# Optimization experiments

Hardware: AMD Instinct MI355X
Metric: run time of the kernel (lower is better)

## Reference

```python
import jax, jax.numpy as jnp
import numpy as np

N = 10000        # nodes
E = 160000       # edges
C = 128          # channel multiplicity (128x0e input)
RBF = 20         # edge_attr_dim
HID = 32         # edge MLP hidden
WN = 3 * C       # tp.weight_numel: 3 uvu paths (0e x Y_l -> l), 128 weights each


def setup_inputs() -> dict:
    key = jax.random.key(0)
    ks = jax.random.split(key, 12)
    f = lambda k, s, sc=1.0: jax.random.normal(k, s, jnp.float32) * sc
    return {
        "node_feat": f(ks[0], (N, C)),
        "edge_attr": f(ks[1], (E, RBF)),
        "edge_rsh": f(ks[2], (E, 9)),
        "edge_index": jax.random.randint(ks[3], (2, E), 0, N),
        # mlp_edge_scalar: Linear(2C->32), Linear(32->WN)
        "Ws1": f(ks[4], (2 * C, HID), 1.0 / np.sqrt(2 * C)), "bs1": jnp.zeros((HID,), jnp.float32),
        "Ws2": f(ks[5], (HID, WN), 1.0 / np.sqrt(HID)), "bs2": jnp.zeros((WN,), jnp.float32),
        # mlp_edge_rbf: Linear(20->32), Linear(32->WN)
        "Wr1": f(ks[6], (RBF, HID), 1.0 / np.sqrt(RBF)), "br1": jnp.zeros((HID,), jnp.float32),
        "Wr2": f(ks[7], (HID, WN), 1.0 / np.sqrt(HID)), "br2": jnp.zeros((WN,), jnp.float32),
        "lin2_w0": f(ks[8], (C, C)), "lin2_b0": jnp.zeros((C,), jnp.float32),
        "lin2_w1": f(ks[9], (C, C)),
        "lin2_w2": f(ks[10], (C, C)),
    }


def reference(node_feat, edge_attr, edge_rsh, edge_index,
              Ws1, bs1, Ws2, bs2, Wr1, br1, Wr2, br2,
              lin2_w0, lin2_b0, lin2_w1, lin2_w2):
    src, dst = edge_index[0], edge_index[1]
    xi = node_feat[src]            # [E, C] gathered scalars (center node)
    xj = node_feat[dst]            # [E, C] gathered scalars (neighbor)

    # First-layer branch: inner_dot of pure scalars -> elementwise product;
    # slice [:, C:] is empty, so s0 = concat(x_i scalars, x_j scalars).
    s0 = jnp.concatenate([xi, xj], axis=-1)  # [E, 2C]

    silu = jax.nn.silu
    w_s = silu(s0 @ Ws1 + bs1) @ Ws2 + bs2            # [E, 3C]
    w_r = silu(edge_attr @ Wr1 + br1) @ Wr2 + br2      # [E, 3C]
    tpw = w_s * w_r                                    # gated tensor-product weights

    w0, w1, w2 = tpw[:, :C], tpw[:, C:2 * C], tpw[:, 2 * C:]
    y0, y1, y2 = edge_rsh[:, :1], edge_rsh[:, 1:4], edge_rsh[:, 4:9]

    # uvu tensor product: per edge, per channel u: w_l[u] * x[u] * Y_l[m]
    m0 = (w0 * xj) * y0                                        # [E, C]
    m1 = (w1 * xj)[:, :, None] * y1[:, None, :]                # [E, C, 3]
    m2 = (w2 * xj)[:, :, None] * y2[:, None, :]                # [E, C, 5]
    msg = jnp.concatenate(
        [m0, m1.reshape(-1, 3 * C), m2.reshape(-1, 5 * C)], axis=-1)  # [E, 9C]

    # scatter-add to destination (edge_index[0])
    accu = jax.ops.segment_sum(msg, src, num_segments=node_feat.shape[0])  # [N, 9C]

    # lin_node2: equivariant linear (per-l channel mixing, bias on scalars only)
    a0 = accu[:, :C]
    a1 = accu[:, C:4 * C].reshape(-1, C, 3)
    a2 = accu[:, 4 * C:].reshape(-1, C, 5)
    inv = 1.0 / np.sqrt(C)  # e3nn o3.Linear fan-in normalization
    o0 = a0 @ lin2_w0 * inv + lin2_b0
    o1 = jnp.einsum('ncm,cd->ndm', a1, lin2_w1) * inv
    o2 = jnp.einsum('ncm,cd->ndm', a2, lin2_w2) * inv
    return jnp.concatenate([o0, o1.reshape(-1, 3 * C), o2.reshape(-1, 5 * C)], axis=-1)
```

## Files before the change

kernel.cpp:

```cpp
#include <hip/hip_runtime.h>
#include <hip/hip_bf16.h>
#include <math.h>

#define NN   10000
#define EE   160000
#define CC   128
#define RBFD 20
#define HIDD 32
#define WND  384
#define MROW 1152
#define EPB  64

typedef _Float16 half2_t __attribute__((ext_vector_type(2)));

__device__ __forceinline__ half2_t u2h(unsigned int u)
{
    union { unsigned int u; half2_t h; } c; c.u = u; return c.h;
}
__device__ __forceinline__ unsigned int pack_h2(float a, float b)
{
    union { half2_t h; unsigned int u; } c;
    c.h.x = (_Float16)a; c.h.y = (_Float16)b; return c.u;
}

__device__ __align__(16) float g_proj[(size_t)NN * 64];
__device__ __align__(16) float g_accu[(size_t)NN * MROW];
__device__ __align__(16) uint4 g_wp[3 * 16 * 64];
__device__ int g_deg[NN];
__device__ int g_offs[NN + 1];
__device__ int g_rel[EE];
__device__ int g_ord[EE];

__device__ __forceinline__ float silu_f(float x) { return x / (1.f + __expf(-x)); }

__global__ __launch_bounds__(256) void zero_kernel()
{
    int tid = blockIdx.x * 256 + threadIdx.x;
    if (tid < NN) g_deg[tid] = 0;
    float4* p = reinterpret_cast<float4*>(g_accu);
    float4 z = make_float4(0.f, 0.f, 0.f, 0.f);
    int n4 = NN * MROW / 4;
    for (int i = tid; i < n4; i += gridDim.x * 256) p[i] = z;
}

__global__ __launch_bounds__(192) void pack_kernel(
    const float* __restrict__ Ws2, const float* __restrict__ Wr2)
{
    int tid = threadIdx.x;
    int sec = tid >> 6, l = tid & 63;
    int c0 = sec * 128 + 2 * l;
    #pragma unroll
    for (int q = 0; q < 4; ++q) {
        unsigned int w0[4], w1[4], r0[4], r1[4];
        #pragma unroll
        for (int i = 0; i < 4; ++i) {
            int p = 4 * q + i;
            int b0 = (2 * p) * WND + c0;
            int b1 = (2 * p + 1) * WND + c0;
            w0[i] = pack_h2(Ws2[b0],     Ws2[b1]);
            w1[i] = pack_h2(Ws2[b0 + 1], Ws2[b1 + 1]);
            r0[i] = pack_h2(Wr2[b0],     Wr2[b1]);
            r1[i] = pack_h2(Wr2[b0 + 1], Wr2[b1 + 1]);
        }
        g_wp[((sec * 16 + 0 * 4 + q) * 64) + l] = make_uint4(w0[0], w0[1], w0[2], w0[3]);
        g_wp[((sec * 16 + 1 * 4 + q) * 64) + l] = make_uint4(w1[0], w1[1], w1[2], w1[3]);
        g_wp[((sec * 16 + 2 * 4 + q) * 64) + l] = make_uint4(r0[0], r0[1], r0[2], r0[3]);
        g_wp[((sec * 16 + 3 * 4 + q) * 64) + l] = make_uint4(r1[0], r1[1], r1[2], r1[3]);
    }
}

__global__ __launch_bounds__(256) void hist_kernel(const int* __restrict__ edge_index)
{
    int e = blockIdx.x * 256 + threadIdx.x;
    if (e < EE) g_rel[e] = atomicAdd(&g_deg[edge_index[e]], 1);
}

__global__ __launch_bounds__(256) void scan_kernel()
{
    __shared__ int sP[256];
    int t = threadIdx.x;
    int lo = t * 40, hi = min(lo + 40, NN);
    int sum = 0;
    for (int i = lo; i < hi; ++i) sum += g_deg[i];
    sP[t] = sum;
    __syncthreads();
    for (int off = 1; off < 256; off <<= 1) {
        int v = (t >= off) ? sP[t - off] : 0;
        __syncthreads();
        sP[t] += v;
        __syncthreads();
    }
    int run = sP[t] - sum;
    if (t == 0) g_offs[0] = 0;
    for (int i = lo; i < hi; ++i) { run += g_deg[i]; g_offs[i + 1] = run; }
}

__global__ __launch_bounds__(256) void proj_kernel(
    const float* __restrict__ nf,
    const float* __restrict__ Ws1, const float* __restrict__ bs1,
    const int* __restrict__ edge_index)
{
    __shared__ float sX[16][132];

    int tid = threadIdx.x;
    int nb = blockIdx.x * 16;

    {
        int eg = blockIdx.x * 256 + tid;
        g_ord[g_offs[edge_index[eg]] + g_rel[eg]] = eg;
    }

    #pragma unroll
    for (int i = tid; i < 512; i += 256) {
        int n = i >> 5, k4 = i & 31;
        float4 v = reinterpret_cast<const float4*>(nf + (size_t)(nb + n) * CC)[k4];
        sX[n][k4 * 4 + 0] = v.x;
        sX[n][k4 * 4 + 1] = v.y;
        sX[n][k4 * 4 + 2] = v.z;
        sX[n][k4 * 4 + 3] = v.w;
    }
    __syncthreads();

    int nl = tid >> 4;
    int qd = tid & 15;
    int j0 = (qd & 7) * 4;
    int rbase = (qd >= 8) ? CC : 0;

    float4 acc;
    if (qd < 8) acc = *reinterpret_cast<const float4*>(&bs1[j0]);
    else        acc = make_float4(0.f, 0.f, 0.f, 0.f);

    const float* wb = Ws1 + (size_t)rbase * HIDD + j0;
    #pragma unroll 4
    for (int k = 0; k < CC; ++k) {
        float f = sX[nl][k];
        float4 w = *reinterpret_cast<const float4*>(wb + (size_t)k * HIDD);
        acc.x = fmaf(f, w.x, acc.x);
        acc.y = fmaf(f, w.y, acc.y);
        acc.z = fmaf(f, w.z, acc.z);
        acc.w = fmaf(f, w.w, acc.w);
    }

    float* o = g_proj + (size_t)(nb + nl) * 64 + ((qd >= 8) ? HIDD : 0) + j0;
    *reinterpret_cast<float4*>(o) = acc;
}

template<int K, int YB, int MOFF>
__device__ __forceinline__ void section_pass(
    int sec, int l,
    const float2* __restrict__ nf2,
    const float* __restrict__ bs2, const float* __restrict__ br2,
    const unsigned int (*__restrict__ sH)[36], const float (*__restrict__ sY)[9],
    const int* __restrict__ sSrc, const int* __restrict__ sDst)
{
    const uint4* wt = g_wp + (size_t)sec * 16 * 64 + l;
    uint4 W0q[4], W1q[4], R0q[4], R1q[4];
    #pragma unroll
    for (int q = 0; q < 4; ++q) {
        W0q[q] = wt[(0 * 4 + q) * 64];
        W1q[q] = wt[(1 * 4 + q) * 64];
        R0q[q] = wt[(2 * 4 + q) * 64];
        R1q[q] = wt[(3 * 4 + q) * 64];
    }

    float2 bsv = *reinterpret_cast<const float2*>(&bs2[sec * 128 + 2 * l]);
    float2 brv = *reinterpret_cast<const float2*>(&br2[sec * 128 + 2 * l]);

    float racc0[K], racc1[K];
    #pragma unroll
    for (int k = 0; k < K; ++k) { racc0[k] = 0.f; racc1[k] = 0.f; }
    int cur = sSrc[0];
    float2 xjn = nf2[(size_t)sDst[0] * 64 + l];

    #pragma unroll 2
    for (int ee = 0; ee < EPB; ++ee) {
        int src = sSrc[ee];
        if (src != cur) {
            float* ab = g_accu + (size_t)cur * MROW + MOFF + 2 * l;
            #pragma unroll
            for (int k = 0; k < K; ++k) {
                unsafeAtomicAdd(ab + k * CC,     racc0[k]);
                unsafeAtomicAdd(ab + k * CC + 1, racc1[k]);
                racc0[k] = 0.f; racc1[k] = 0.f;
            }
            cur = src;
        }
        float2 xj = xjn;
        xjn = nf2[(size_t)sDst[(ee + 1) & (EPB - 1)] * 64 + l];
        const uint4* hp = reinterpret_cast<const uint4*>(&sH[ee][0]);
        float as0 = bsv.x, as1 = bsv.y, ar0 = brv.x, ar1 = brv.y;
        #pragma unroll
        for (int q = 0; q < 4; ++q) {
            uint4 hv = hp[q];
            uint4 rv = hp[4 + q];
            as0 = __builtin_amdgcn_fdot2(u2h(hv.x), u2h(W0q[q].x), as0, false);
            as1 = __builtin_amdgcn_fdot2(u2h(hv.x), u2h(W1q[q].x), as1, false);
            as0 = __builtin_amdgcn_fdot2(u2h(hv.y), u2h(W0q[q].y), as0, false);
            as1 = __builtin_amdgcn_fdot2(u2h(hv.y), u2h(W1q[q].y), as1, false);
            as0 = __builtin_amdgcn_fdot2(u2h(hv.z), u2h(W0q[q].z), as0, false);
            as1 = __builtin_amdgcn_fdot2(u2h(hv.z), u2h(W1q[q].z), as1, false);
            as0 = __builtin_amdgcn_fdot2(u2h(hv.w), u2h(W0q[q].w), as0, false);
            as1 = __builtin_amdgcn_fdot2(u2h(hv.w), u2h(W1q[q].w), as1, false);
            ar0 = __builtin_amdgcn_fdot2(u2h(rv.x), u2h(R0q[q].x), ar0, false);
            ar1 = __builtin_amdgcn_fdot2(u2h(rv.x), u2h(R1q[q].x), ar1, false);
            ar0 = __builtin_amdgcn_fdot2(u2h(rv.y), u2h(R0q[q].y), ar0, false);
            ar1 = __builtin_amdgcn_fdot2(u2h(rv.y), u2h(R1q[q].y), ar1, false);
            ar0 = __builtin_amdgcn_fdot2(u2h(rv.z), u2h(R0q[q].z), ar0, false);
            ar1 = __builtin_amdgcn_fdot2(u2h(rv.z), u2h(R1q[q].z), ar1, false);
            ar0 = __builtin_amdgcn_fdot2(u2h(rv.w), u2h(R0q[q].w), ar0, false);
            ar1 = __builtin_amdgcn_fdot2(u2h(rv.w), u2h(R1q[q].w), ar1, false);
        }
        float u0 = as0 * ar0 * xj.x;
        float u1 = as1 * ar1 * xj.y;
        #pragma unroll
        for (int k = 0; k < K; ++k) {
            float yv = sY[ee][YB + k];
            racc0[k] = fmaf(u0, yv, racc0[k]);
            racc1[k] = fmaf(u1, yv, racc1[k]);
        }
    }
    float* ab = g_accu + (size_t)cur * MROW + MOFF + 2 * l;
    #pragma unroll
    for (int k = 0; k < K; ++k) {
        unsafeAtomicAdd(ab + k * CC,     racc0[k]);
        unsafeAtomicAdd(ab + k * CC + 1, racc1[k]);
    }
}

__global__ __launch_bounds__(192, 4) void fused_kernel(
    const float* __restrict__ nf,
    const float* __restrict__ edge_attr,
    const float* __restrict__ edge_rsh,
    const int*   __restrict__ edge_index,
    const float* __restrict__ bs2,
    const float* __restrict__ Wr1, const float* __restrict__ br1,
    const float* __restrict__ br2)
{
    __shared__ unsigned int sH[EPB][36];
    __shared__ float sY[EPB][9];
    __shared__ int   sSrc[EPB], sDst[EPB];

    int tid = threadIdx.x;
    int w = tid / 64;
    int l = tid & 63;
    int p = blockIdx.x * EPB + l;
    int e = g_ord[p];

    if (w == 0) {
        int s = edge_index[e];
        int t = edge_index[EE + e];
        const float4* pi = reinterpret_cast<const float4*>(g_proj + (size_t)s * 64);
        const float4* pj = reinterpret_cast<const float4*>(g_proj + (size_t)t * 64 + HIDD);
        #pragma unroll
        for (int j4 = 0; j4 < HIDD / 8; ++j4) {
            float4 a0 = pi[2 * j4],     b0 = pj[2 * j4];
            float4 a1 = pi[2 * j4 + 1], b1 = pj[2 * j4 + 1];
            sH[l][4 * j4 + 0] = pack_h2(silu_f(a0.x + b0.x), silu_f(a0.y + b0.y));
            sH[l][4 * j4 + 1] = pack_h2(silu_f(a0.z + b0.z), silu_f(a0.w + b0.w));
            sH[l][4 * j4 + 2] = pack_h2(silu_f(a1.x + b1.x), silu_f(a1.y + b1.y));
            sH[l][4 * j4 + 3] = pack_h2(silu_f(a1.z + b1.z), silu_f(a1.w + b1.w));
        }
        sSrc[l] = s;
        sDst[l] = t;
    } else if (w == 1) {
        float hr[HIDD];
        #pragma unroll
        for (int j = 0; j < HIDD; ++j) hr[j] = br1[j];
        #pragma unroll 1
        for (int k4 = 0; k4 < RBFD / 4; ++k4) {
            float4 a = reinterpret_cast<const float4*>(edge_attr + (size_t)e * RBFD)[k4];
            const float* wp = Wr1 + (4 * k4) * HIDD;
            #pragma unroll
            for (int j = 0; j < HIDD; ++j) {
                hr[j] = fmaf(a.x, wp[j], hr[j]);
                hr[j] = fmaf(a.y, wp[HIDD + j], hr[j]);
                hr[j] = fmaf(a.z, wp[2 * HIDD + j], hr[j]);
                hr[j] = fmaf(a.w, wp[3 * HIDD + j], hr[j]);
            }
        }
        #pragma unroll
        for (int pp = 0; pp < 16; ++pp)
            sH[l][16 + pp] = pack_h2(silu_f(hr[2 * pp]), silu_f(hr[2 * pp + 1]));
    } else {
        #pragma unroll
        for (int i = 0; i < 9; ++i) sY[l][i] = edge_rsh[(size_t)e * 9 + i];
    }
    __syncthreads();

    const float2* nf2 = reinterpret_cast<const float2*>(nf);
    if (w == 0)
        section_pass<1, 0, 0>     (0, l, nf2, bs2, br2, sH, sY, sSrc, sDst);
    else if (w == 1)
        section_pass<3, 1, CC>    (1, l, nf2, bs2, br2, sH, sY, sSrc, sDst);
    else
        section_pass<5, 4, 4 * CC>(2, l, nf2, bs2, br2, sH, sY, sSrc, sDst);
}

__global__ __launch_bounds__(256) void lin2_kernel(
    const float* __restrict__ W0, const float* __restrict__ b0,
    const float* __restrict__ W1, const float* __restrict__ W2,
    float* __restrict__ out)
{
    __shared__ float sA[8 * MROW];
    int n0 = blockIdx.x * 8;
    const float4* g = reinterpret_cast<const float4*>(g_accu + (size_t)n0 * MROW);
    for (int i = threadIdx.x; i < 8 * MROW / 4; i += 256)
        reinterpret_cast<float4*>(sA)[i] = g[i];
    __syncthreads();

    int d  = threadIdx.x & (CC - 1);
    int nl = threadIdx.x >> 7;

    float acc[4][9];
    #pragma unroll
    for (int q = 0; q < 4; ++q)
        #pragma unroll
        for (int m = 0; m < 9; ++m) acc[q][m] = 0.f;

    #pragma unroll 1
    for (int c = 0; c < CC; ++c) {
        float w0 = W0[c * CC + d];
        float w1 = W1[c * CC + d];
        float w2 = W2[c * CC + d];
        #pragma unroll
        for (int q = 0; q < 4; ++q) {
            const float* a = sA + (size_t)(nl * 4 + q) * MROW;
            acc[q][0] = fmaf(a[c],          w0, acc[q][0]);
            acc[q][1] = fmaf(a[CC + c],     w1, acc[q][1]);
            acc[q][2] = fmaf(a[2 * CC + c], w1, acc[q][2]);
            acc[q][3] = fmaf(a[3 * CC + c], w1, acc[q][3]);
            acc[q][4] = fmaf(a[4 * CC + c], w2, acc[q][4]);
            acc[q][5] = fmaf(a[5 * CC + c], w2, acc[q][5]);
            acc[q][6] = fmaf(a[6 * CC + c], w2, acc[q][6]);
            acc[q][7] = fmaf(a[7 * CC + c], w2, acc[q][7]);
            acc[q][8] = fmaf(a[8 * CC + c], w2, acc[q][8]);
        }
    }

    const float inv = 0.08838834764831845f;
    #pragma unroll
    for (int q = 0; q < 4; ++q) {
        size_t ob = (size_t)(n0 + nl * 4 + q) * MROW;
        out[ob + d] = acc[q][0] * inv + b0[d];
        #pragma unroll
        for (int m = 0; m < 3; ++m) out[ob + CC + d * 3 + m]     = acc[q][1 + m] * inv;
        #pragma unroll
        for (int m = 0; m < 5; ++m) out[ob + 4 * CC + d * 5 + m] = acc[q][4 + m] * inv;
    }
}

extern "C" void kernel_launch(void* const* d_in, const int* in_sizes, int n_in,
                              void* d_out, int out_size, void* d_ws, size_t ws_size,
                              hipStream_t stream)
{
    const float* node_feat  = (const float*)d_in[0];
    const float* edge_attr  = (const float*)d_in[1];
    const float* edge_rsh   = (const float*)d_in[2];
    const int*   edge_index = (const int*)  d_in[3];
    const float* Ws1 = (const float*)d_in[4];
    const float* bs1 = (const float*)d_in[5];
    const float* Ws2 = (const float*)d_in[6];
    const float* bs2 = (const float*)d_in[7];
    const float* Wr1 = (const float*)d_in[8];
    const float* br1 = (const float*)d_in[9];
    const float* Wr2 = (const float*)d_in[10];
    const float* br2 = (const float*)d_in[11];
    const float* W0  = (const float*)d_in[12];
    const float* b0  = (const float*)d_in[13];
    const float* W1  = (const float*)d_in[14];
    const float* W2  = (const float*)d_in[15];
    float* out = (float*)d_out;

    zero_kernel<<<2048, 256, 0, stream>>>();
    pack_kernel<<<1, 192, 0, stream>>>(Ws2, Wr2);
    hist_kernel<<<EE / 256, 256, 0, stream>>>(edge_index);
    scan_kernel<<<1, 256, 0, stream>>>();
    proj_kernel<<<NN / 16, 256, 0, stream>>>(node_feat, Ws1, bs1, edge_index);
    fused_kernel<<<EE / EPB, 192, 0, stream>>>(
        node_feat, edge_attr, edge_rsh, edge_index,
        bs2, Wr1, br1, br2);
    lin2_kernel<<<NN / 8, 256, 0, stream>>>(W0, b0, W1, W2, out);
}
```

Measured before the change: 283.7 us.

## Drop zero kernel by clearing accumulator in lin2, vectorize lin2 LDS reads

```diff
diff --git a/kernel.cpp b/kernel.cpp
--- a/kernel.cpp
+++ b/kernel.cpp
@@ -33,20 +33,11 @@
 
 __device__ __forceinline__ float silu_f(float x) { return x / (1.f + __expf(-x)); }
 
-__global__ __launch_bounds__(256) void zero_kernel()
-{
-    int tid = blockIdx.x * 256 + threadIdx.x;
-    if (tid < NN) g_deg[tid] = 0;
-    float4* p = reinterpret_cast<float4*>(g_accu);
-    float4 z = make_float4(0.f, 0.f, 0.f, 0.f);
-    int n4 = NN * MROW / 4;
-    for (int i = tid; i < n4; i += gridDim.x * 256) p[i] = z;
-}
-
 __global__ __launch_bounds__(192) void pack_kernel(
     const float* __restrict__ Ws2, const float* __restrict__ Wr2)
 {
     int tid = threadIdx.x;
+    for (int i = tid; i < NN; i += 192) g_deg[i] = 0;
     int sec = tid >> 6, l = tid & 63;
     int c0 = sec * 128 + 2 * l;
     #pragma unroll
@@ -303,9 +294,13 @@
 {
     __shared__ float sA[8 * MROW];
     int n0 = blockIdx.x * 8;
-    const float4* g = reinterpret_cast<const float4*>(g_accu + (size_t)n0 * MROW);
-    for (int i = threadIdx.x; i < 8 * MROW / 4; i += 256)
-        reinterpret_cast<float4*>(sA)[i] = g[i];
+    float4* g = reinterpret_cast<float4*>(g_accu + (size_t)n0 * MROW);
+    const float4 z4 = make_float4(0.f, 0.f, 0.f, 0.f);
+    for (int i = threadIdx.x; i < 8 * MROW / 4; i += 256) {
+        float4 v = g[i];
+        reinterpret_cast<float4*>(sA)[i] = v;
+        g[i] = z4;
+    }
     __syncthreads();
 
     int d  = threadIdx.x & (CC - 1);
@@ -318,22 +313,32 @@
         for (int m = 0; m < 9; ++m) acc[q][m] = 0.f;
 
     #pragma unroll 1
-    for (int c = 0; c < CC; ++c) {
-        float w0 = W0[c * CC + d];
-        float w1 = W1[c * CC + d];
-        float w2 = W2[c * CC + d];
+    for (int c4 = 0; c4 < CC / 4; ++c4) {
+        float w0c[4], w1c[4], w2c[4];
+        #pragma unroll
+        for (int cc = 0; cc < 4; ++cc) {
+            int c = 4 * c4 + cc;
+            w0c[cc] = W0[c * CC + d];
+            w1c[cc] = W1[c * CC + d];
+            w2c[cc] = W2[c * CC + d];
+        }
         #pragma unroll
         for (int q = 0; q < 4; ++q) {
-            const float* a = sA + (size_t)(nl * 4 + q) * MROW;
-            acc[q][0] = fmaf(a[c],          w0, acc[q][0]);
-            acc[q][1] = fmaf(a[CC + c],     w1, acc[q][1]);
-            acc[q][2] = fmaf(a[2 * CC + c], w1, acc[q][2]);
-            acc[q][3] = fmaf(a[3 * CC + c], w1, acc[q][3]);
-            acc[q][4] = fmaf(a[4 * CC + c], w2, acc[q][4]);
-            acc[q][5] = fmaf(a[5 * CC + c], w2, acc[q][5]);
-            acc[q][6] = fmaf(a[6 * CC + c], w2, acc[q][6]);
-            acc[q][7] = fmaf(a[7 * CC + c], w2, acc[q][7]);
-            acc[q][8] = fmaf(a[8 * CC + c], w2, acc[q][8]);
+            const float* a = sA + (size_t)(nl * 4 + q) * MROW + 4 * c4;
+            float4 am[9];
+            #pragma unroll
+            for (int m = 0; m < 9; ++m)
+                am[m] = *reinterpret_cast<const float4*>(a + m * CC);
+            #pragma unroll
+            for (int cc = 0; cc < 4; ++cc) {
+                acc[q][0] = fmaf((&am[0].x)[cc], w0c[cc], acc[q][0]);
+                #pragma unroll
+                for (int m = 1; m < 4; ++m)
+                    acc[q][m] = fmaf((&am[m].x)[cc], w1c[cc], acc[q][m]);
+                #pragma unroll
+                for (int m = 4; m < 9; ++m)
+                    acc[q][m] = fmaf((&am[m].x)[cc], w2c[cc], acc[q][m]);
+            }
         }
     }
 
@@ -371,7 +376,6 @@
     const float* W2  = (const float*)d_in[15];
     float* out = (float*)d_out;
 
-    zero_kernel<<<2048, 256, 0, stream>>>();
     pack_kernel<<<1, 192, 0, stream>>>(Ws2, Wr2);
     hist_kernel<<<EE / 256, 256, 0, stream>>>(edge_index);
     scan_kernel<<<1, 256, 0, stream>>>();
```

New measurement: 247.2 us. 1.15x faster.
